# Optimization experiments

Hardware: AMD Instinct MI355X
Metric: run time of the kernel (lower is better)

## Reference

```python
import jax, jax.numpy as jnp
import numpy as np

DIM = 1024
NUM_HEADS = 16
HEAD_DIM = DIM // NUM_HEADS
SCALE = HEAD_DIM ** -0.5
B, N = 2, 2048


def setup_inputs() -> dict:
    key = jax.random.key(0)
    k_x, k_qkv, k_prjw, k_prjb = jax.random.split(key, 4)
    # nn.Linear(dim, 3*dim, bias=False): weight [3*dim, dim]
    s = 1.0 / np.sqrt(DIM)
    return {
        "x": jax.random.normal(k_x, (B, N, DIM), dtype=jnp.float32),
        "w_qkv": jax.random.uniform(k_qkv, (3 * DIM, DIM), jnp.float32, -s, s),
        "w_prj": jax.random.uniform(k_prjw, (DIM, DIM), jnp.float32, -s, s),
        "b_prj": jax.random.uniform(k_prjb, (DIM,), jnp.float32, -s, s),
    }


def reference(x, w_qkv, w_prj, b_prj):
    Bb, Nn, C = x.shape
    qkv = jnp.einsum("bnc,dc->bnd", x, w_qkv)            # [B,N,3C]
    qkv = qkv.reshape(Bb, Nn, 3, NUM_HEADS, HEAD_DIM)
    qkv = jnp.transpose(qkv, (2, 0, 3, 1, 4))            # [3,B,H,N,hd]
    q, k, v = qkv[0], qkv[1], qkv[2]
    attn = jnp.einsum("bhqd,bhkd->bhqk", q, k) * SCALE   # [B,H,N,N]
    attn = jax.nn.softmax(attn, axis=-1)
    out = jnp.einsum("bhqk,bhkd->bhqd", attn, v)         # [B,H,N,hd]
    out = jnp.transpose(out, (0, 2, 1, 3)).reshape(Bb, Nn, C)
    # dropout layers are identity at eval / p=0
    return jnp.einsum("bnc,dc->bnd", out, w_prj) + b_prj
```

## Files before the change

### kernel.cpp

```cpp
#include <hip/hip_runtime.h>

typedef unsigned short u16;
typedef unsigned int u32;
typedef __attribute__((ext_vector_type(8))) short s16x8;
typedef __attribute__((ext_vector_type(4))) short s16x4;
typedef __attribute__((ext_vector_type(4))) float f32x4;

#define DIM    1024
#define NHEADS 16
#define HD     64
#define NSEQ   2048
#define QKVN   3072

__device__ __forceinline__ u16 f2bf(float f) {
  u32 u = __float_as_uint(f);
  u += 0x7FFF + ((u >> 16) & 1);
  return (u16)(u >> 16);
}

__device__ __forceinline__ float vexp2(float x) {
#if __has_builtin(__builtin_amdgcn_exp2f)
  return __builtin_amdgcn_exp2f(x);
#else
  return __expf(x * 0.69314718055994531f);
#endif
}

__device__ __forceinline__ void async16(const u16* g, u16* l) {
  __builtin_amdgcn_global_load_lds(
      (const __attribute__((address_space(1))) unsigned int*)g,
      (__attribute__((address_space(3))) unsigned int*)l, 16, 0, 0);
}

__global__ void cast_all(const float* __restrict__ x, const float* __restrict__ wq,
                         const float* __restrict__ wp, u16* __restrict__ xo,
                         u16* __restrict__ wqo, u16* __restrict__ wpo) {
  int i = blockIdx.x * 256 + threadIdx.x;
  const float4* src; u16* dst; int off;
  if (i < 1048576)      { src = (const float4*)x;  dst = xo;  off = i; }
  else if (i < 1835008) { src = (const float4*)wq; dst = wqo; off = i - 1048576; }
  else                  { src = (const float4*)wp; dst = wpo; off = i - 1835008; }
  float4 f = src[off];
  ushort4 o;
  o.x = f2bf(f.x); o.y = f2bf(f.y); o.z = f2bf(f.z); o.w = f2bf(f.w);
  ((ushort4*)dst)[off] = o;
}

template <bool FINAL>
__global__ __launch_bounds__(256, 3) void gemm_bt(
    const u16* __restrict__ A, const u16* __restrict__ Bw, u16* __restrict__ qkv,
    u16* __restrict__ vt, const float* __restrict__ bias, float* __restrict__ outp) {
  constexpr int K = 1024;
  constexpr int BM = 128;
  constexpr int BN = FINAL ? 64 : 128;
  constexpr int MT = 32;
  constexpr int IT = 4;
  constexpr int JT = FINAL ? 2 : 4;
  constexpr int ACALLS = BM / 16;
  constexpr int BCALLS = BN / 16;
  constexpr int TCALLS = ACALLS + BCALLS;
  constexpr int PW = TCALLS / 4;
  const float QS = 0.18033688011112042f;
  const int bm = blockIdx.x % MT;
  const int bn = blockIdx.x / MT;
  const int tid = threadIdx.x;
  const int wave = tid >> 6, lane = tid & 63;
  const int q4 = lane >> 4, l15 = lane & 15;
  const int wm = wave >> 1, wn = wave & 1;
  const int m0 = bm * BM, n0 = bn * BN;

  __shared__ alignas(16) u16 lsA[2][BM * 32];
  __shared__ alignas(16) u16 lsB[2][BN * 32];

  f32x4 acc[IT][JT];
#pragma unroll
  for (int i = 0; i < IT; i++)
#pragma unroll
    for (int j = 0; j < JT; j++) acc[i][j] = (f32x4){0.f, 0.f, 0.f, 0.f};

  auto stage = [&](int k0, int buf) {
#pragma unroll
    for (int j = 0; j < PW; ++j) {
      int t = wave * PW + j;
      if (t < ACALLS) {
        int lin = t * 64 + lane;
        int r = lin >> 2, c = lin & 3;
        async16(A + (size_t)(m0 + r) * K + k0 + c * 8, lsA[buf] + t * 512);
      } else {
        int tb = t - ACALLS;
        int lin = tb * 64 + lane;
        int r = lin >> 2, c = lin & 3;
        async16(Bw + (size_t)(n0 + r) * K + k0 + c * 8, lsB[buf] + tb * 512);
      }
    }
  };

  stage(0, 0);

  for (int k0 = 0; k0 < K; k0 += 32) {
    const int buf = (k0 >> 5) & 1;
    __syncthreads();
    if (k0 + 32 < K) stage(k0 + 32, buf ^ 1);
    s16x8 af[IT], bfr[JT];
#pragma unroll
    for (int i = 0; i < IT; ++i)
      af[i] = *(const s16x8*)(lsA[buf] + (wm * (IT * 16) + i * 16 + l15) * 32 + q4 * 8);
#pragma unroll
    for (int j = 0; j < JT; ++j)
      bfr[j] = *(const s16x8*)(lsB[buf] + (wn * (JT * 16) + j * 16 + l15) * 32 + q4 * 8);
    __builtin_amdgcn_s_setprio(1);
#pragma unroll
    for (int i = 0; i < IT; ++i)
#pragma unroll
      for (int j = 0; j < JT; ++j)
        acc[i][j] = __builtin_amdgcn_mfma_f32_16x16x32_bf16(af[i], bfr[j], acc[i][j], 0, 0, 0);
    __builtin_amdgcn_s_setprio(0);
  }

#pragma unroll
  for (int i = 0; i < IT; i++) {
#pragma unroll
    for (int j = 0; j < JT; j++) {
      int n = n0 + wn * (JT * 16) + j * 16 + l15;
      int mb = m0 + wm * (IT * 16) + i * 16 + q4 * 4;
      if (FINAL) {
#pragma unroll
        for (int r = 0; r < 4; r++)
          outp[(size_t)(mb + r) * DIM + n] = acc[i][j][r] + bias[n];
      } else if (n < 2048) {
        float sc = (n < 1024) ? QS : 1.0f;
#pragma unroll
        for (int r = 0; r < 4; r++)
          qkv[(size_t)(mb + r) * QKVN + n] = f2bf(acc[i][j][r] * sc);
      } else {
        int b = mb >> 11, tok = mb & 2047;
        int h = (n >> 6) & 15, hd = n & 63;
        ushort4 pk;
        pk.x = f2bf(acc[i][j][0]); pk.y = f2bf(acc[i][j][1]);
        pk.z = f2bf(acc[i][j][2]); pk.w = f2bf(acc[i][j][3]);
        *(ushort4*)(vt + ((size_t)((b * NHEADS + h) * HD + hd)) * NSEQ + tok) = pk;
      }
    }
  }
}

__global__ __launch_bounds__(256, 2) void attn_kernel(const u16* __restrict__ qkv,
                                                      const u16* __restrict__ vt,
                                                      u16* __restrict__ aout) {
  const int blk = blockIdx.x;
  const int bh = blk & 31, qt = blk >> 5;
  const int b = bh >> 4, h = bh & 15;
  const int tid = threadIdx.x;
  const int wave = tid >> 6, lane = tid & 63;
  const int g = wave >> 1, wq = wave & 1;
  const int q4 = lane >> 4, l15 = lane & 15;

  __shared__ alignas(16) u16 smem[32768];
  u16* lsKb = smem + g * 2 * 4096;
  u16* lsVb = smem + 16384 + g * 2 * 4096;

  s16x8 aq[4][2];
#pragma unroll
  for (int rt = 0; rt < 4; ++rt)
#pragma unroll
    for (int kc = 0; kc < 2; ++kc) {
      int row = b * NSEQ + qt * 128 + wq * 64 + rt * 16 + l15;
      aq[rt][kc] = *(const s16x8*)(qkv + (size_t)row * QKVN + h * HD + kc * 32 + q4 * 8);
    }

  f32x4 o[4][4];
  f32x4 osum[4];
  const s16x8 vones8 = {(short)0x3F80, (short)0x3F80, (short)0x3F80, (short)0x3F80,
                        (short)0x3F80, (short)0x3F80, (short)0x3F80, (short)0x3F80};
#pragma unroll
  for (int rt = 0; rt < 4; ++rt) {
    osum[rt] = (f32x4){0.f, 0.f, 0.f, 0.f};
#pragma unroll
    for (int ht = 0; ht < 4; ++ht) o[rt][ht] = (f32x4){0.f, 0.f, 0.f, 0.f};
  }

  auto stage = [&](int ktl, int buf) {
#pragma unroll
    for (int j = 0; j < 4; ++j) {
      int t = wq * 4 + j;
      int lin = t * 64 + lane;
      int r = lin >> 3, c = (lin & 7) ^ (r & 7);
      int key = g * 1024 + ktl * 64;
      async16(qkv + (size_t)(b * NSEQ + key + r) * QKVN + DIM + h * HD + c * 8,
              lsKb + buf * 4096 + t * 512);
      async16(vt + (size_t)(bh * HD + r) * NSEQ + key + c * 8,
              lsVb + buf * 4096 + t * 512);
    }
  };

  stage(0, 0);

  for (int kt = 0; kt < 16; ++kt) {
    const int buf = kt & 1;
    __syncthreads();
    if (kt + 1 < 16) stage(kt + 1, buf ^ 1);
    const u16* lsK = lsKb + buf * 4096;
    const u16* lsV = lsVb + buf * 4096;

    s16x8 kf[2][4];
#pragma unroll
    for (int kc = 0; kc < 2; ++kc)
#pragma unroll
      for (int ct = 0; ct < 4; ++ct) {
        int r = ct * 16 + l15;
        int c = (kc * 4 + q4) ^ (r & 7);
        kf[kc][ct] = *(const s16x8*)(lsK + r * 64 + c * 8);
      }
    s16x8 vf8[2][4];
#pragma unroll
    for (int c = 0; c < 2; ++c)
#pragma unroll
      for (int ht = 0; ht < 4; ++ht) {
        int row = ht * 16 + l15;
        int ch0 = c * 4 + (q4 >> 1);
        int ch1 = ch0 + 2;
        union { s16x4 hh[2]; s16x8 v; } u;
        u.hh[0] = *(const s16x4*)(lsV + row * 64 + (ch0 ^ (row & 7)) * 8 + (q4 & 1) * 4);
        u.hh[1] = *(const s16x4*)(lsV + row * 64 + (ch1 ^ (row & 7)) * 8 + (q4 & 1) * 4);
        vf8[c][ht] = u.v;
      }

#pragma unroll
    for (int rt = 0; rt < 4; ++rt) {
      f32x4 st[4];
#pragma unroll
      for (int ct = 0; ct < 4; ++ct) st[ct] = (f32x4){0.f, 0.f, 0.f, 0.f};
      __builtin_amdgcn_s_setprio(1);
#pragma unroll
      for (int kc = 0; kc < 2; ++kc)
#pragma unroll
        for (int ct = 0; ct < 4; ++ct)
          st[ct] = __builtin_amdgcn_mfma_f32_16x16x32_bf16(kf[kc][ct], aq[rt][kc], st[ct], 0, 0, 0);
      __builtin_amdgcn_s_setprio(0);

      s16x8 pa8[2];
#pragma unroll
      for (int c = 0; c < 2; ++c) {
        union { u32 w[4]; s16x8 v; } pk;
#pragma unroll
        for (int h2 = 0; h2 < 2; ++h2) {
          int ct = c * 2 + h2;
          u32 u0 = __float_as_uint(vexp2(st[ct][0]));
          u32 u1 = __float_as_uint(vexp2(st[ct][1]));
          u32 u2 = __float_as_uint(vexp2(st[ct][2]));
          u32 u3 = __float_as_uint(vexp2(st[ct][3]));
          pk.w[h2 * 2 + 0] = (u0 >> 16) | (u1 & 0xffff0000u);
          pk.w[h2 * 2 + 1] = (u2 >> 16) | (u3 & 0xffff0000u);
        }
        pa8[c] = pk.v;
      }

      __builtin_amdgcn_s_setprio(1);
#pragma unroll
      for (int c = 0; c < 2; ++c) {
        osum[rt] = __builtin_amdgcn_mfma_f32_16x16x32_bf16(pa8[c], vones8, osum[rt], 0, 0, 0);
#pragma unroll
        for (int ht = 0; ht < 4; ++ht)
          o[rt][ht] = __builtin_amdgcn_mfma_f32_16x16x32_bf16(pa8[c], vf8[c][ht], o[rt][ht], 0, 0, 0);
      }
      __builtin_amdgcn_s_setprio(0);
    }
  }

  float* lsOa = (float*)smem;
  float* lsOb = lsOa + 32 * 132;
  float* lsS0 = lsOa + 64 * 132;
  float* lsS1 = lsS0 + 128;

  __syncthreads();
  if (g == 1) {
#pragma unroll
    for (int rt = 0; rt < 4; ++rt) {
      int a0 = l15 * 132 + wq * 64 + rt * 16 + q4 * 4;
      *(float4*)(lsOa + a0)            = (float4){o[rt][0][0], o[rt][0][1], o[rt][0][2], o[rt][0][3]};
      *(float4*)(lsOa + a0 + 16 * 132) = (float4){o[rt][1][0], o[rt][1][1], o[rt][1][2], o[rt][1][3]};
      if (l15 == 0) {
#pragma unroll
        for (int r = 0; r < 4; ++r)
          lsS1[wq * 64 + rt * 16 + q4 * 4 + r] = osum[rt][r];
      }
    }
  } else {
#pragma unroll
    for (int rt = 0; rt < 4; ++rt) {
      int a0 = l15 * 132 + wq * 64 + rt * 16 + q4 * 4;
      *(float4*)(lsOb + a0)            = (float4){o[rt][2][0], o[rt][2][1], o[rt][2][2], o[rt][2][3]};
      *(float4*)(lsOb + a0 + 16 * 132) = (float4){o[rt][3][0], o[rt][3][1], o[rt][3][2], o[rt][3][3]};
      if (l15 == 0) {
#pragma unroll
        for (int r = 0; r < 4; ++r)
          lsS0[wq * 64 + rt * 16 + q4 * 4 + r] = osum[rt][r];
      }
    }
  }
  __syncthreads();
  if (g == 0) {
#pragma unroll
    for (int rt = 0; rt < 4; ++rt) {
      float4 s2 = *(const float4*)(lsS1 + wq * 64 + rt * 16 + q4 * 4);
      float inv[4];
      inv[0] = 1.0f / (osum[rt][0] + s2.x);
      inv[1] = 1.0f / (osum[rt][1] + s2.y);
      inv[2] = 1.0f / (osum[rt][2] + s2.z);
      inv[3] = 1.0f / (osum[rt][3] + s2.w);
      int a0 = l15 * 132 + wq * 64 + rt * 16 + q4 * 4;
      float4 p0 = *(const float4*)(lsOa + a0);
      float4 p1 = *(const float4*)(lsOa + a0 + 16 * 132);
      float v0[4] = {o[rt][0][0] + p0.x, o[rt][0][1] + p0.y, o[rt][0][2] + p0.z, o[rt][0][3] + p0.w};
      float v1[4] = {o[rt][1][0] + p1.x, o[rt][1][1] + p1.y, o[rt][1][2] + p1.z, o[rt][1][3] + p1.w};
#pragma unroll
      for (int r = 0; r < 4; ++r) {
        int n = qt * 128 + wq * 64 + rt * 16 + q4 * 4 + r;
        size_t base = (size_t)(b * NSEQ + n) * DIM + h * HD;
        aout[base + 0  + l15] = f2bf(v0[r] * inv[r]);
        aout[base + 16 + l15] = f2bf(v1[r] * inv[r]);
      }
    }
  } else {
#pragma unroll
    for (int rt = 0; rt < 4; ++rt) {
      float4 s2 = *(const float4*)(lsS0 + wq * 64 + rt * 16 + q4 * 4);
      float inv[4];
      inv[0] = 1.0f / (osum[rt][0] + s2.x);
      inv[1] = 1.0f / (osum[rt][1] + s2.y);
      inv[2] = 1.0f / (osum[rt][2] + s2.z);
      inv[3] = 1.0f / (osum[rt][3] + s2.w);
      int a0 = l15 * 132 + wq * 64 + rt * 16 + q4 * 4;
      float4 p2 = *(const float4*)(lsOb + a0);
      float4 p3 = *(const float4*)(lsOb + a0 + 16 * 132);
      float v2[4] = {o[rt][2][0] + p2.x, o[rt][2][1] + p2.y, o[rt][2][2] + p2.z, o[rt][2][3] + p2.w};
      float v3[4] = {o[rt][3][0] + p3.x, o[rt][3][1] + p3.y, o[rt][3][2] + p3.z, o[rt][3][3] + p3.w};
#pragma unroll
      for (int r = 0; r < 4; ++r) {
        int n = qt * 128 + wq * 64 + rt * 16 + q4 * 4 + r;
        size_t base = (size_t)(b * NSEQ + n) * DIM + h * HD;
        aout[base + 32 + l15] = f2bf(v2[r] * inv[r]);
        aout[base + 48 + l15] = f2bf(v3[r] * inv[r]);
      }
    }
  }
}

extern "C" void kernel_launch(void* const* d_in, const int* in_sizes, int n_in,
                              void* d_out, int out_size, void* d_ws, size_t ws_size,
                              hipStream_t stream) {
  const float* x     = (const float*)d_in[0];
  const float* w_qkv = (const float*)d_in[1];
  const float* w_prj = (const float*)d_in[2];
  const float* b_prj = (const float*)d_in[3];
  float* out = (float*)d_out;

  char* ws = (char*)d_ws;
  u16* x_bf    = (u16*)(ws);
  u16* wqkv_bf = (u16*)(ws + (size_t)(8u << 20));
  u16* wprj_bf = (u16*)(ws + (size_t)(14u << 20));
  u16* qkv     = (u16*)(ws + (size_t)(16u << 20));
  u16* vt      = (u16*)(ws + (size_t)(40u << 20));
  u16* aout    = (u16*)(ws + (size_t)(48u << 20));

  cast_all<<<8192, 256, 0, stream>>>(x, w_qkv, w_prj, x_bf, wqkv_bf, wprj_bf);
  gemm_bt<false><<<32 * 24, 256, 0, stream>>>(x_bf, wqkv_bf, qkv, vt, nullptr, nullptr);
  attn_kernel<<<512, 256, 0, stream>>>(qkv, vt, aout);
  gemm_bt<true><<<32 * 16, 256, 0, stream>>>(aout, wprj_bf, nullptr, nullptr, b_prj, out);
}
```

Before: 168.0 us.

## Stage V transpose through swizzled LDS for coalesced stores; grid-stride cast kernel

New measurement: 168.8 us. Within noise of the previous version (+0.5%).

```diff
diff --git a/kernel.cpp b/kernel.cpp
--- a/kernel.cpp
+++ b/kernel.cpp
@@ -35,15 +35,16 @@
 __global__ void cast_all(const float* __restrict__ x, const float* __restrict__ wq,
                          const float* __restrict__ wp, u16* __restrict__ xo,
                          u16* __restrict__ wqo, u16* __restrict__ wpo) {
-  int i = blockIdx.x * 256 + threadIdx.x;
-  const float4* src; u16* dst; int off;
-  if (i < 1048576)      { src = (const float4*)x;  dst = xo;  off = i; }
-  else if (i < 1835008) { src = (const float4*)wq; dst = wqo; off = i - 1048576; }
-  else                  { src = (const float4*)wp; dst = wpo; off = i - 1835008; }
-  float4 f = src[off];
-  ushort4 o;
-  o.x = f2bf(f.x); o.y = f2bf(f.y); o.z = f2bf(f.z); o.w = f2bf(f.w);
-  ((ushort4*)dst)[off] = o;
+  for (int i = blockIdx.x * 256 + threadIdx.x; i < 2097152; i += 2048 * 256) {
+    const float4* src; u16* dst; int off;
+    if (i < 1048576)      { src = (const float4*)x;  dst = xo;  off = i; }
+    else if (i < 1835008) { src = (const float4*)wq; dst = wqo; off = i - 1048576; }
+    else                  { src = (const float4*)wp; dst = wpo; off = i - 1835008; }
+    float4 f = src[off];
+    ushort4 o;
+    o.x = f2bf(f.x); o.y = f2bf(f.y); o.z = f2bf(f.z); o.w = f2bf(f.w);
+    ((ushort4*)dst)[off] = o;
+  }
 }
 
 template <bool FINAL>
@@ -69,8 +70,9 @@
   const int wm = wave >> 1, wn = wave & 1;
   const int m0 = bm * BM, n0 = bn * BN;
 
-  __shared__ alignas(16) u16 lsA[2][BM * 32];
-  __shared__ alignas(16) u16 lsB[2][BN * 32];
+  __shared__ alignas(16) u16 sm[2 * BM * 32 + 2 * BN * 32];
+  u16* lsA_ = sm;
+  u16* lsB_ = sm + 2 * BM * 32;
 
   f32x4 acc[IT][JT];
 #pragma unroll
@@ -85,12 +87,12 @@
       if (t < ACALLS) {
         int lin = t * 64 + lane;
         int r = lin >> 2, c = lin & 3;
-        async16(A + (size_t)(m0 + r) * K + k0 + c * 8, lsA[buf] + t * 512);
+        async16(A + (size_t)(m0 + r) * K + k0 + c * 8, lsA_ + buf * BM * 32 + t * 512);
       } else {
         int tb = t - ACALLS;
         int lin = tb * 64 + lane;
         int r = lin >> 2, c = lin & 3;
-        async16(Bw + (size_t)(n0 + r) * K + k0 + c * 8, lsB[buf] + tb * 512);
+        async16(Bw + (size_t)(n0 + r) * K + k0 + c * 8, lsB_ + buf * BN * 32 + tb * 512);
       }
     }
   };
@@ -104,10 +106,10 @@
     s16x8 af[IT], bfr[JT];
 #pragma unroll
     for (int i = 0; i < IT; ++i)
-      af[i] = *(const s16x8*)(lsA[buf] + (wm * (IT * 16) + i * 16 + l15) * 32 + q4 * 8);
+      af[i] = *(const s16x8*)(lsA_ + buf * BM * 32 + (wm * (IT * 16) + i * 16 + l15) * 32 + q4 * 8);
 #pragma unroll
     for (int j = 0; j < JT; ++j)
-      bfr[j] = *(const s16x8*)(lsB[buf] + (wn * (JT * 16) + j * 16 + l15) * 32 + q4 * 8);
+      bfr[j] = *(const s16x8*)(lsB_ + buf * BN * 32 + (wn * (JT * 16) + j * 16 + l15) * 32 + q4 * 8);
     __builtin_amdgcn_s_setprio(1);
 #pragma unroll
     for (int i = 0; i < IT; ++i)
@@ -117,29 +119,51 @@
     __builtin_amdgcn_s_setprio(0);
   }
 
-#pragma unroll
-  for (int i = 0; i < IT; i++) {
-#pragma unroll
-    for (int j = 0; j < JT; j++) {
-      int n = n0 + wn * (JT * 16) + j * 16 + l15;
-      int mb = m0 + wm * (IT * 16) + i * 16 + q4 * 4;
-      if (FINAL) {
-#pragma unroll
-        for (int r = 0; r < 4; r++)
-          outp[(size_t)(mb + r) * DIM + n] = acc[i][j][r] + bias[n];
-      } else if (n < 2048) {
-        float sc = (n < 1024) ? QS : 1.0f;
-#pragma unroll
-        for (int r = 0; r < 4; r++)
-          qkv[(size_t)(mb + r) * QKVN + n] = f2bf(acc[i][j][r] * sc);
-      } else {
-        int b = mb >> 11, tok = mb & 2047;
-        int h = (n >> 6) & 15, hd = n & 63;
+  if (FINAL || n0 < 2048) {
+#pragma unroll
+    for (int i = 0; i < IT; i++) {
+#pragma unroll
+      for (int j = 0; j < JT; j++) {
+        int n = n0 + wn * (JT * 16) + j * 16 + l15;
+        int mb = m0 + wm * (IT * 16) + i * 16 + q4 * 4;
+        if (FINAL) {
+#pragma unroll
+          for (int r = 0; r < 4; r++)
+            outp[(size_t)(mb + r) * DIM + n] = acc[i][j][r] + bias[n];
+        } else {
+          float sc = (n < 1024) ? QS : 1.0f;
+#pragma unroll
+          for (int r = 0; r < 4; r++)
+            qkv[(size_t)(mb + r) * QKVN + n] = f2bf(acc[i][j][r] * sc);
+        }
+      }
+    }
+  } else {
+    __syncthreads();
+    u16* tt = sm;
+#pragma unroll
+    for (int i = 0; i < IT; i++) {
+#pragma unroll
+      for (int j = 0; j < JT; j++) {
+        int vcol = wn * (JT * 16) + j * 16 + l15;
+        int tokb = wm * (IT * 16) + i * 16 + q4 * 4;
+        int p = tokb ^ ((vcol & 7) << 3);
         ushort4 pk;
         pk.x = f2bf(acc[i][j][0]); pk.y = f2bf(acc[i][j][1]);
         pk.z = f2bf(acc[i][j][2]); pk.w = f2bf(acc[i][j][3]);
-        *(ushort4*)(vt + ((size_t)((b * NHEADS + h) * HD + hd)) * NSEQ + tok) = pk;
-      }
+        *(ushort4*)(tt + vcol * 128 + p) = pk;
+      }
+    }
+    __syncthreads();
+    int vcol = tid >> 1;
+    int sw = (vcol & 7) << 3;
+    size_t vbase = ((size_t)((m0 >> 11) * (NHEADS * HD) + (n0 - 2048) + vcol)) * NSEQ
+                   + (m0 & 2047);
+#pragma unroll
+    for (int k = 0; k < 8; ++k) {
+      int T = ((tid & 1) * 8 + k) * 8;
+      uint4 v = *(const uint4*)(tt + vcol * 128 + (T ^ sw));
+      *(uint4*)(vt + vbase + T) = v;
     }
   }
 }
@@ -363,7 +387,7 @@
   u16* vt      = (u16*)(ws + (size_t)(40u << 20));
   u16* aout    = (u16*)(ws + (size_t)(48u << 20));
 
-  cast_all<<<8192, 256, 0, stream>>>(x, w_qkv, w_prj, x_bf, wqkv_bf, wprj_bf);
+  cast_all<<<2048, 256, 0, stream>>>(x, w_qkv, w_prj, x_bf, wqkv_bf, wprj_bf);
   gemm_bt<false><<<32 * 24, 256, 0, stream>>>(x_bf, wqkv_bf, qkv, vt, nullptr, nullptr);
   attn_kernel<<<512, 256, 0, stream>>>(qkv, vt, aout);
   gemm_bt<true><<<32 * 16, 256, 0, stream>>>(aout, wprj_bf, nullptr, nullptr, b_prj, out);
```
